# Kernel optimization log

Hardware: AMD Instinct MI355X
Metric: run time of the kernel (lower is better)

Reference implementation:

```python
import jax, jax.numpy as jnp
import numpy as np

B, S, E, H = 4, 2048, 1024, 16
D = E // H  # head_size = 64

def setup_inputs() -> dict:
    key = jax.random.key(0)
    ks = jax.random.split(key, 10)
    s_e = E ** -0.5
    s_4e = (4 * E) ** -0.5
    inp = {
        "x": jax.random.normal(ks[0], (B, S, E), dtype=jnp.float32),
        # per-head Q/K/V weights, stacked: [H, E, D], no bias
        "Wq": jax.random.normal(ks[1], (H, E, D), dtype=jnp.float32) * s_e,
        "Wk": jax.random.normal(ks[2], (H, E, D), dtype=jnp.float32) * s_e,
        "Wv": jax.random.normal(ks[3], (H, E, D), dtype=jnp.float32) * s_e,
        "Wo": jax.random.normal(ks[4], (E, E), dtype=jnp.float32) * s_e,
        "bo": jax.random.normal(ks[5], (E,), dtype=jnp.float32) * 0.01,
        "W1": jax.random.normal(ks[6], (E, 4 * E), dtype=jnp.float32) * s_e,
        "b1": jax.random.normal(ks[7], (4 * E,), dtype=jnp.float32) * 0.01,
        "W2": jax.random.normal(ks[8], (4 * E, E), dtype=jnp.float32) * s_4e,
        "b2": jax.random.normal(ks[9], (E,), dtype=jnp.float32) * 0.01,
    }
    return inp

def reference(x, Wq, Wk, Wv, Wo, bo, W1, b1, W2, b2):
    b, s, e = x.shape
    # NOTE: original scales by embedding_size**-0.5 (Size of x), not head_size
    scale = e ** -0.5
    q = jnp.einsum("bse,hed->bhsd", x, Wq)
    k = jnp.einsum("bse,hed->bhsd", x, Wk)
    v = jnp.einsum("bse,hed->bhsd", x, Wv)
    scores = jnp.einsum("bhsd,bhtd->bhst", q, k) * scale
    causal = jnp.tril(jnp.ones((s, s), dtype=bool))
    scores = jnp.where(causal, scores, -jnp.inf)
    weights = jax.nn.softmax(scores, axis=-1)
    attn = jnp.einsum("bhst,bhtd->bhsd", weights, v)  # [B,H,S,D]
    # concat heads along last dim: [B,S,H*D]
    attn = attn.transpose(0, 2, 1, 3).reshape(b, s, e)
    y = attn @ Wo + bo
    x = x + y  # residual (no LayerNorm applied in original forward)
    h = jax.nn.relu(x @ W1 + b1)
    ffn = h @ W2 + b2
    return x + ffn
```

## Files before the change

kernel.cpp:

```cpp
#include <hip/hip_runtime.h>
#include <stdint.h>

#define B_ 4
#define S_ 2048
#define E_ 1024
#define H_ 16
#define D_ 64

typedef unsigned short u16;
typedef u16 u16x8 __attribute__((ext_vector_type(8)));
typedef __bf16 bf16x8 __attribute__((ext_vector_type(8)));
typedef float f32x4 __attribute__((ext_vector_type(4)));

__device__ __forceinline__ float bf2f(u16 x) {
  unsigned int v = ((unsigned int)x) << 16;
  return __builtin_bit_cast(float, v);
}
__device__ __forceinline__ u16 f2bf(float f) {
  unsigned int u = __builtin_bit_cast(unsigned int, f);
  unsigned int r = (u + 0x7fffu + ((u >> 16) & 1u)) >> 16;
  return (u16)r;
}

__device__ __forceinline__ void gl2lds16(const u16* g, u16* l) {
  __builtin_amdgcn_global_load_lds(
      (const __attribute__((address_space(1))) void*)g,
      (__attribute__((address_space(3))) void*)l, 16, 0, 0);
}

__global__ __launch_bounds__(256) void cast_bf16_k(const float* __restrict__ src,
                                                   u16* __restrict__ dst, long n) {
  long i = ((long)blockIdx.x * 256 + threadIdx.x) * 8;
  if (i + 8 <= n) {
    f32x4 a = *(const f32x4*)(src + i), b = *(const f32x4*)(src + i + 4);
    u16x8 o;
#pragma unroll
    for (int j = 0; j < 4; j++) { o[j] = f2bf(a[j]); o[j + 4] = f2bf(b[j]); }
    *(u16x8*)(dst + i) = o;
  }
}

__global__ __launch_bounds__(256) void castT_k(const float* __restrict__ src,
                                               u16* __restrict__ dst, int R, int C) {
  long bofs = (long)blockIdx.z * R * C;
  src += bofs; dst += bofs;
  __shared__ u16 t[32][33];
  int c0 = blockIdx.x * 32, r0 = blockIdx.y * 32;
  int lc = threadIdx.x & 31, lr8 = threadIdx.x >> 5;
#pragma unroll
  for (int i = 0; i < 4; i++) {
    int lr = lr8 + i * 8;
    t[lr][lc] = f2bf(src[(long)(r0 + lr) * C + c0 + lc]);
  }
  __syncthreads();
#pragma unroll
  for (int i = 0; i < 4; i++) {
    int lr = lr8 + i * 8;
    dst[(long)(c0 + lr) * R + r0 + lc] = t[lc][lr];
  }
}

__global__ __launch_bounds__(256) void vT_k(const u16* __restrict__ QKV,
                                            u16* __restrict__ VTg) {
  int bh = blockIdx.z, d0 = blockIdx.y * 32, t0 = blockIdx.x * 32;
  int b = bh >> 4, h = bh & 15;
  __shared__ u16 t[32][33];
  int lc = threadIdx.x & 31, lr8 = threadIdx.x >> 5;
#pragma unroll
  for (int i = 0; i < 4; i++) {
    int lr = lr8 + i * 8;
    t[lr][lc] = QKV[(long)(b * S_ + t0 + lr) * 3072 + 2048 + h * 64 + d0 + lc];
  }
  __syncthreads();
#pragma unroll
  for (int i = 0; i < 4; i++) {
    int lr = lr8 + i * 8;
    VTg[((long)bh * 64 + d0 + lr) * S_ + t0 + lc] = t[lc][lr];
  }
}

template <bool AF32, bool CF32>
__global__ __launch_bounds__(256) void gemm128(const void* __restrict__ Av,
                                               const u16* __restrict__ BT,
                                               void* __restrict__ Cv,
                                               const float* __restrict__ bias,
                                               const float* __restrict__ resid,
                                               int M, int N, int K, int relu,
                                               u16* __restrict__ Cbf) {
  __shared__ u16 As[128 * 32];
  __shared__ u16 Bs[128 * 32];
  const int tid = threadIdx.x;
  const int wave = tid >> 6, lane = tid & 63;
  const int m0 = blockIdx.y * 128, n0 = blockIdx.x * 128;
  const int wm = wave >> 1, wn = wave & 1;
  const int fr = lane & 15, quad = lane >> 4;

  f32x4 acc[4][4] = {};

  const int srow = wave * 32 + (lane >> 2);
  const int skcol = (lane & 3) * 8;

  for (int k0 = 0; k0 < K; k0 += 32) {
    __syncthreads();
    if (AF32) {
      const float* Ap = (const float*)Av + (long)(m0 + (tid >> 1)) * K + k0 + (tid & 1) * 16;
      f32x4 f0 = *(const f32x4*)Ap, f1 = *(const f32x4*)(Ap + 4);
      f32x4 f2 = *(const f32x4*)(Ap + 8), f3 = *(const f32x4*)(Ap + 12);
      u16x8 p0, p1;
#pragma unroll
      for (int j = 0; j < 4; j++) {
        p0[j] = f2bf(f0[j]); p0[j + 4] = f2bf(f1[j]);
        p1[j] = f2bf(f2[j]); p1[j + 4] = f2bf(f3[j]);
      }
      *(u16x8*)&As[(tid >> 1) * 32 + (tid & 1) * 16] = p0;
      *(u16x8*)&As[(tid >> 1) * 32 + (tid & 1) * 16 + 8] = p1;
    } else {
      const u16* Ag = (const u16*)Av + (long)(m0 + srow) * K + k0 + skcol;
      gl2lds16(Ag, &As[(wave * 32) * 32]);
      gl2lds16(Ag + 16 * (long)K, &As[(wave * 32 + 16) * 32]);
    }
    {
      const u16* Bg = BT + (long)(n0 + srow) * K + k0 + skcol;
      gl2lds16(Bg, &Bs[(wave * 32) * 32]);
      gl2lds16(Bg + 16 * (long)K, &Bs[(wave * 32 + 16) * 32]);
    }
    __syncthreads();

    bf16x8 af[4], bfr[4];
#pragma unroll
    for (int mi = 0; mi < 4; mi++)
      af[mi] = __builtin_bit_cast(bf16x8, *(const u16x8*)&As[(wm * 64 + mi * 16 + fr) * 32 + quad * 8]);
#pragma unroll
    for (int ni = 0; ni < 4; ni++)
      bfr[ni] = __builtin_bit_cast(bf16x8, *(const u16x8*)&Bs[(wn * 64 + ni * 16 + fr) * 32 + quad * 8]);
#pragma unroll
    for (int mi = 0; mi < 4; mi++)
#pragma unroll
      for (int ni = 0; ni < 4; ni++)
        acc[mi][ni] = __builtin_amdgcn_mfma_f32_16x16x32_bf16(af[mi], bfr[ni], acc[mi][ni], 0, 0, 0);
  }

#pragma unroll
  for (int mi = 0; mi < 4; mi++)
#pragma unroll
    for (int ni = 0; ni < 4; ni++)
#pragma unroll
      for (int r = 0; r < 4; r++) {
        int gm = m0 + wm * 64 + mi * 16 + quad * 4 + r;
        int gn = n0 + wn * 64 + ni * 16 + fr;
        float v = acc[mi][ni][r];
        if (bias) v += bias[gn];
        if (resid) v += resid[(long)gm * N + gn];
        if (relu) v = fmaxf(v, 0.f);
        if (CF32) ((float*)Cv)[(long)gm * N + gn] = v;
        else      ((u16*)Cv)[(long)gm * N + gn] = f2bf(v);
        if (Cbf) Cbf[(long)gm * N + gn] = f2bf(v);
      }
}

__device__ __forceinline__ bf16x8 ldfrag32(const u16* base, int r, int quad) {
  int u = (r * 32 + quad * 8) ^ (((r >> 3) & 1) << 4);
  return __builtin_bit_cast(bf16x8, *(const u16x8*)(base + u));
}

__device__ __forceinline__ void stage_tile(const u16* __restrict__ A,
                                           const u16* __restrict__ BT, int K,
                                           int m0, int n0, int k0,
                                           u16* __restrict__ buf,
                                           int sr_, int sc_, int wbase) {
#pragma unroll
  for (int h = 0; h < 2; h++) {
    int r = h * 128 + sr_;
    int c = sc_ ^ (((r >> 3) & 1) << 4);
    gl2lds16(A + (size_t)(m0 + r) * K + k0 + c, buf + h * 4096 + wbase);
  }
  int c = sc_ ^ (((sr_ >> 3) & 1) << 4);
  gl2lds16(BT + (size_t)(n0 + sr_) * K + k0 + c, buf + 8192 + wbase);
}

template <bool CF32>
__global__ __launch_bounds__(512) void gemm3b(const u16* __restrict__ A,
                                              const u16* __restrict__ BT,
                                              void* __restrict__ Cv,
                                              const float* __restrict__ bias,
                                              const float* __restrict__ resid,
                                              int M, int N, int K, int relu,
                                              u16* __restrict__ Cbf) {
  (void)M;
  constexpr int BM = 256, BN = 128, BK = 32;
  constexpr int AU = BM * BK;
  constexpr int BUF = AU + BN * BK;

  __shared__ u16 sm[3 * BUF];
  const int tid = threadIdx.x;
  const int wave = tid >> 6, lane = tid & 63;
  const int wm = wave >> 1, wn = wave & 1;
  const int fr = lane & 15, quad = lane >> 4;

  const int nbx = gridDim.x;
  const int nwg = nbx * (int)gridDim.y;
  const int wgid = blockIdx.y * nbx + blockIdx.x;
  const int qq = nwg >> 3, rr = nwg & 7;
  const int xcd = wgid & 7, loc = wgid >> 3;
  const int sw = (xcd < rr ? xcd * (qq + 1) : rr * (qq + 1) + (xcd - rr) * qq) + loc;
  const int n0 = (sw % nbx) * BN;
  const int m0 = (sw / nbx) * BM;

  const int NT = K / BK;

  f32x4 acc[4][4] = {};

  const int sc_ = (tid & 3) * 8;
  const int sr_ = tid >> 2;
  const int wbase = wave << 9;

  const int rA = wm * 64 + fr;
  const int rB = wn * 64 + fr;

  stage_tile(A, BT, K, m0, n0, 0, sm, sr_, sc_, wbase);
  if (NT > 1) {
    stage_tile(A, BT, K, m0, n0, BK, sm + BUF, sr_, sc_, wbase);
    asm volatile("s_waitcnt vmcnt(3)" ::: "memory");
  } else {
    asm volatile("s_waitcnt vmcnt(0)" ::: "memory");
  }
  __builtin_amdgcn_s_barrier();

  int cur = 0;
  for (int t = 0; t < NT; ++t) {
    u16* cb = sm + cur * BUF;

    if (t + 2 < NT) {
      int s2 = cur + 2; if (s2 >= 3) s2 -= 3;
      stage_tile(A, BT, K, m0, n0, (t + 2) * BK, sm + s2 * BUF, sr_, sc_, wbase);
    }

    bf16x8 aF[4], bF[4];
#pragma unroll
    for (int mi = 0; mi < 4; ++mi) aF[mi] = ldfrag32(cb, rA + mi * 16, quad);
#pragma unroll
    for (int ni = 0; ni < 4; ++ni) bF[ni] = ldfrag32(cb + AU, rB + ni * 16, quad);

    asm volatile("s_waitcnt lgkmcnt(0)" ::: "memory");
    __builtin_amdgcn_sched_barrier(0);
    __builtin_amdgcn_s_setprio(1);
#pragma unroll
    for (int mi = 0; mi < 4; ++mi)
#pragma unroll
      for (int ni = 0; ni < 4; ++ni)
        acc[mi][ni] = __builtin_amdgcn_mfma_f32_16x16x32_bf16(aF[mi], bF[ni], acc[mi][ni], 0, 0, 0);
    __builtin_amdgcn_s_setprio(0);

    if (t + 2 < NT) asm volatile("s_waitcnt vmcnt(3)" ::: "memory");
    else            asm volatile("s_waitcnt vmcnt(0)" ::: "memory");
    __builtin_amdgcn_s_barrier();
    cur = cur + 1; if (cur >= 3) cur -= 3;
  }

#pragma unroll
  for (int mi = 0; mi < 4; ++mi)
#pragma unroll
    for (int ni = 0; ni < 4; ++ni)
#pragma unroll
      for (int r = 0; r < 4; ++r) {
        int gm = m0 + wm * 64 + mi * 16 + quad * 4 + r;
        int gn = n0 + wn * 64 + ni * 16 + fr;
        float v = acc[mi][ni][r];
        if (bias) v += bias[gn];
        if (resid) v += resid[(long)gm * N + gn];
        if (relu) v = fmaxf(v, 0.f);
        if (CF32) ((float*)Cv)[(long)gm * N + gn] = v;
        else      ((u16*)Cv)[(long)gm * N + gn] = f2bf(v);
        if (Cbf) Cbf[(long)gm * N + gn] = f2bf(v);
      }
}

__global__ __launch_bounds__(256) void attn_mfma3(const u16* __restrict__ QKV,
                                                  const u16* __restrict__ VTg,
                                                  u16* __restrict__ attn) {
  int p = blockIdx.x, h = blockIdx.y, b = blockIdx.z;
  int tid = threadIdx.x;
  int wq = tid >> 6, lane = tid & 63;
  int fr = lane & 15, quad = lane >> 4;
  int kf = quad * 8;

  __shared__ u16 Qs[64][72];
  __shared__ u16 Ks[64][72];
  __shared__ u16 Vt[64][72];
  __shared__ u16 Ps[4][16][72];

  const u16* base = QKV + (long)b * S_ * 3072;
  const u16* vbase = VTg + (long)(b * 16 + h) * 64 * S_;
  int st = tid >> 2;
  int sd = (tid & 3) * 16;

  for (int ti = 0; ti < 2; ti++) {
    int qt = ti ? (31 - p) : p;

    {
      const u16* qr = base + (long)(qt * 64 + st) * 3072 + h * 64 + sd;
      u16x8 a = *(const u16x8*)qr, d = *(const u16x8*)(qr + 8);
      u16x8 oa, od;
#pragma unroll
      for (int j = 0; j < 8; j++) {
        oa[j] = f2bf(bf2f(a[j]) * 0.03125f);
        od[j] = f2bf(bf2f(d[j]) * 0.03125f);
      }
      *(u16x8*)&Qs[st][sd] = oa;
      *(u16x8*)&Qs[st][sd + 8] = od;
    }
    __syncthreads();
    bf16x8 qf0 = __builtin_bit_cast(bf16x8, *(const u16x8*)&Qs[wq * 16 + fr][kf]);
    bf16x8 qf1 = __builtin_bit_cast(bf16x8, *(const u16x8*)&Qs[wq * 16 + fr][32 + kf]);

    f32x4 acc[4] = {};
    float l[4] = {0.f, 0.f, 0.f, 0.f};

    for (int c = 0; c <= qt; c++) {
      int t0 = c * 64;
      __syncthreads();
      {
        const u16* kr = base + (long)(t0 + st) * 3072 + 1024 + h * 64 + sd;
        u16x8 k0 = *(const u16x8*)kr, k1 = *(const u16x8*)(kr + 8);
        const u16* vr = vbase + (long)st * S_ + t0 + sd;
        u16x8 v0 = *(const u16x8*)vr, v1 = *(const u16x8*)(vr + 8);
        *(u16x8*)&Ks[st][sd] = k0;
        *(u16x8*)&Ks[st][sd + 8] = k1;
        *(u16x8*)&Vt[st][sd] = v0;
        *(u16x8*)&Vt[st][sd + 8] = v1;
      }
      __syncthreads();

      f32x4 sc[4] = {};
#pragma unroll
      for (int nt = 0; nt < 4; nt++) {
        bf16x8 b0 = __builtin_bit_cast(bf16x8, *(const u16x8*)&Ks[nt * 16 + fr][kf]);
        bf16x8 b1 = __builtin_bit_cast(bf16x8, *(const u16x8*)&Ks[nt * 16 + fr][32 + kf]);
        sc[nt] = __builtin_amdgcn_mfma_f32_16x16x32_bf16(qf0, b0, sc[nt], 0, 0, 0);
        sc[nt] = __builtin_amdgcn_mfma_f32_16x16x32_bf16(qf1, b1, sc[nt], 0, 0, 0);
      }

      if (c == qt) {
        int qloc = wq * 16 + quad * 4;
#pragma unroll
        for (int nt = 0; nt < 4; nt++)
#pragma unroll
          for (int r = 0; r < 4; r++)
            if (nt * 16 + fr > qloc + r) sc[nt][r] = -1e30f;
      }

#pragma unroll
      for (int nt = 0; nt < 4; nt++)
#pragma unroll
        for (int r = 0; r < 4; r++) {
          float pv = __expf(sc[nt][r]);
          sc[nt][r] = pv;
          l[r] += pv;
        }

#pragma unroll
      for (int nt = 0; nt < 4; nt++)
#pragma unroll
        for (int r = 0; r < 4; r++)
          Ps[wq][quad * 4 + r][nt * 16 + fr] = f2bf(sc[nt][r]);

      bf16x8 pa0 = __builtin_bit_cast(bf16x8, *(const u16x8*)&Ps[wq][fr][kf]);
      bf16x8 pa1 = __builtin_bit_cast(bf16x8, *(const u16x8*)&Ps[wq][fr][32 + kf]);
#pragma unroll
      for (int nt = 0; nt < 4; nt++) {
        bf16x8 vb0 = __builtin_bit_cast(bf16x8, *(const u16x8*)&Vt[nt * 16 + fr][kf]);
        bf16x8 vb1 = __builtin_bit_cast(bf16x8, *(const u16x8*)&Vt[nt * 16 + fr][32 + kf]);
        acc[nt] = __builtin_amdgcn_mfma_f32_16x16x32_bf16(pa0, vb0, acc[nt], 0, 0, 0);
        acc[nt] = __builtin_amdgcn_mfma_f32_16x16x32_bf16(pa1, vb1, acc[nt], 0, 0, 0);
      }
    }

#pragma unroll
    for (int r = 0; r < 4; r++)
#pragma unroll
      for (int off = 1; off < 16; off <<= 1) l[r] += __shfl_xor(l[r], off);

    long row = (long)b * S_ + qt * 64 + wq * 16 + quad * 4;
#pragma unroll
    for (int nt = 0; nt < 4; nt++)
#pragma unroll
      for (int r = 0; r < 4; r++)
        attn[(row + r) * 1024 + h * 64 + nt * 16 + fr] = f2bf(acc[nt][r] / l[r]);
  }
}

extern "C" void kernel_launch(void* const* d_in, const int* in_sizes, int n_in,
                              void* d_out, int out_size, void* d_ws, size_t ws_size,
                              hipStream_t stream) {
  (void)in_sizes; (void)n_in; (void)out_size;
  const float* x  = (const float*)d_in[0];
  const float* Wq = (const float*)d_in[1];
  const float* Wk = (const float*)d_in[2];
  const float* Wv = (const float*)d_in[3];
  const float* Wo = (const float*)d_in[4];
  const float* bo = (const float*)d_in[5];
  const float* W1 = (const float*)d_in[6];
  const float* b1 = (const float*)d_in[7];
  const float* W2 = (const float*)d_in[8];
  const float* b2 = (const float*)d_in[9];
  float* out = (float*)d_out;

  char* ws = (char*)d_ws;
  u16*   QKV  = (u16*)(ws);
  u16*   attn = (u16*)(ws + 50331648);
  u16*   hbuf = (u16*)(ws);
  float* x1   = (float*)(ws + 67108864);
  u16*   VTg  = (u16*)(ws + 67108864);
  u16*   xb   = (u16*)(ws + 83886080);
  u16*   WT   = (u16*)(ws + 100663296);
  u16*   WoT  = (u16*)(ws + 106954752);
  u16*   W1T  = (u16*)(ws + 109051904);
  u16*   W2T  = (u16*)(ws + 117440512);
  u16*   x1b  = (u16*)(ws + 125829120);
  bool bigws = ws_size >= (size_t)142606336;

  cast_bf16_k<<<4096, 256, 0, stream>>>(x, xb, (long)8192 * 1024);
  castT_k<<<dim3(2, 32, 16), 256, 0, stream>>>(Wq, WT, 1024, 64);
  castT_k<<<dim3(2, 32, 16), 256, 0, stream>>>(Wk, WT + 1048576, 1024, 64);
  castT_k<<<dim3(2, 32, 16), 256, 0, stream>>>(Wv, WT + 2097152, 1024, 64);
  castT_k<<<dim3(32, 32, 1), 256, 0, stream>>>(Wo, WoT, 1024, 1024);
  castT_k<<<dim3(128, 32, 1), 256, 0, stream>>>(W1, W1T, 1024, 4096);
  castT_k<<<dim3(32, 128, 1), 256, 0, stream>>>(W2, W2T, 4096, 1024);

  gemm3b<false><<<dim3(24, 32), 512, 0, stream>>>(xb, WT, QKV, nullptr, nullptr, 8192, 3072, 1024, 0, nullptr);
  vT_k<<<dim3(64, 2, 64), 256, 0, stream>>>(QKV, VTg);
  attn_mfma3<<<dim3(16, H_, B_), 256, 0, stream>>>(QKV, VTg, attn);
  gemm3b<true><<<dim3(8, 32), 512, 0, stream>>>(attn, WoT, x1, bo, x, 8192, 1024, 1024, 0, bigws ? x1b : nullptr);
  if (bigws)
    gemm3b<false><<<dim3(32, 32), 512, 0, stream>>>(x1b, W1T, hbuf, b1, nullptr, 8192, 4096, 1024, 1, nullptr);
  else
    gemm128<true, false><<<dim3(32, 64), 256, 0, stream>>>(x1, W1T, hbuf, b1, nullptr, 8192, 4096, 1024, 1, nullptr);
  gemm3b<true><<<dim3(8, 32), 512, 0, stream>>>(hbuf, W2T, out, b2, x1, 8192, 1024, 4096, 0, nullptr);
}
```

Baseline: 534.4 us.

## Add 128x128 triple-buffered GEMM and swizzle attention LDS with exp2 softmax

Adds a new 256-thread GEMM kernel with 128x128 tiles, BK=32, triple-buffered async global-to-LDS staging, XCD-aware block remapping and an XOR-swizzled LDS layout. It replaces the 512-thread gemm3b for the QKV, output-projection and W2 GEMMs, giving more, smaller workgroups. The attention kernel switches from padded LDS arrays to XOR-swizzled 64-wide rows to avoid bank conflicts, and folds log2(e) into the Q scale so exp2f can be used. It also fuses the P store into the exp loop. The smaller tiles trade per-block data reuse for higher occupancy and better load balance.

```diff
diff --git a/kernel.cpp b/kernel.cpp
--- a/kernel.cpp
+++ b/kernel.cpp
@@ -275,6 +275,124 @@
       }
 }
 
+__device__ __forceinline__ void stage_tile_s(const u16* __restrict__ A,
+                                             const u16* __restrict__ BT, int K,
+                                             int m0, int n0, int k0,
+                                             u16* __restrict__ buf,
+                                             int sr_, int sc_, int wbase) {
+#pragma unroll
+  for (int h = 0; h < 2; h++) {
+    int r = h * 64 + sr_;
+    int c = sc_ ^ (((r >> 3) & 1) << 4);
+    gl2lds16(A + (size_t)(m0 + r) * K + k0 + c, buf + h * 2048 + wbase);
+  }
+#pragma unroll
+  for (int h = 0; h < 2; h++) {
+    int r = h * 64 + sr_;
+    int c = sc_ ^ (((r >> 3) & 1) << 4);
+    gl2lds16(BT + (size_t)(n0 + r) * K + k0 + c, buf + 4096 + h * 2048 + wbase);
+  }
+}
+
+template <bool CF32>
+__global__ __launch_bounds__(256) void gemm3s(const u16* __restrict__ A,
+                                              const u16* __restrict__ BT,
+                                              void* __restrict__ Cv,
+                                              const float* __restrict__ bias,
+                                              const float* __restrict__ resid,
+                                              int M, int N, int K, int relu,
+                                              u16* __restrict__ Cbf) {
+  (void)M;
+  constexpr int BM = 128, BN = 128, BK = 32;
+  constexpr int AU = BM * BK;
+  constexpr int BUF = 2 * AU;
+
+  __shared__ u16 sm[3 * BUF];
+  const int tid = threadIdx.x;
+  const int wave = tid >> 6, lane = tid & 63;
+  const int wm = wave >> 1, wn = wave & 1;
+  const int fr = lane & 15, quad = lane >> 4;
+
+  const int nbx = gridDim.x;
+  const int nwg = nbx * (int)gridDim.y;
+  const int wgid = blockIdx.y * nbx + blockIdx.x;
+  const int qq = nwg >> 3, rr = nwg & 7;
+  const int xcd = wgid & 7, loc = wgid >> 3;
+  const int sw = (xcd < rr ? xcd * (qq + 1) : rr * (qq + 1) + (xcd - rr) * qq) + loc;
+  const int n0 = (sw % nbx) * BN;
+  const int m0 = (sw / nbx) * BM;
+
+  const int NT = K / BK;
+
+  f32x4 acc[4][4] = {};
+
+  const int sc_ = (tid & 3) * 8;
+  const int sr_ = tid >> 2;
+  const int wbase = wave << 9;
+
+  const int rA = wm * 64 + fr;
+  const int rB = wn * 64 + fr;
+
+  stage_tile_s(A, BT, K, m0, n0, 0, sm, sr_, sc_, wbase);
+  if (NT > 1) {
+    stage_tile_s(A, BT, K, m0, n0, BK, sm + BUF, sr_, sc_, wbase);
+    asm volatile("s_waitcnt vmcnt(4)" ::: "memory");
+  } else {
+    asm volatile("s_waitcnt vmcnt(0)" ::: "memory");
+  }
+  __builtin_amdgcn_s_barrier();
+
+  int cur = 0;
+  for (int t = 0; t < NT; ++t) {
+    u16* cb = sm + cur * BUF;
+
+    if (t + 2 < NT) {
+      int s2 = cur + 2; if (s2 >= 3) s2 -= 3;
+      stage_tile_s(A, BT, K, m0, n0, (t + 2) * BK, sm + s2 * BUF, sr_, sc_, wbase);
+    }
+
+    bf16x8 aF[4], bF[4];
+#pragma unroll
+    for (int mi = 0; mi < 4; ++mi) aF[mi] = ldfrag32(cb, rA + mi * 16, quad);
+#pragma unroll
+    for (int ni = 0; ni < 4; ++ni) bF[ni] = ldfrag32(cb + AU, rB + ni * 16, quad);
+
+    asm volatile("s_waitcnt lgkmcnt(0)" ::: "memory");
+    __builtin_amdgcn_sched_barrier(0);
+    __builtin_amdgcn_s_setprio(1);
+#pragma unroll
+    for (int mi = 0; mi < 4; ++mi)
+#pragma unroll
+      for (int ni = 0; ni < 4; ++ni)
+        acc[mi][ni] = __builtin_amdgcn_mfma_f32_16x16x32_bf16(aF[mi], bF[ni], acc[mi][ni], 0, 0, 0);
+    __builtin_amdgcn_s_setprio(0);
+
+    if (t + 2 < NT) asm volatile("s_waitcnt vmcnt(4)" ::: "memory");
+    else            asm volatile("s_waitcnt vmcnt(0)" ::: "memory");
+    __builtin_amdgcn_s_barrier();
+    cur = cur + 1; if (cur >= 3) cur -= 3;
+  }
+
+#pragma unroll
+  for (int mi = 0; mi < 4; ++mi)
+#pragma unroll
+    for (int ni = 0; ni < 4; ++ni)
+#pragma unroll
+      for (int r = 0; r < 4; ++r) {
+        int gm = m0 + wm * 64 + mi * 16 + quad * 4 + r;
+        int gn = n0 + wn * 64 + ni * 16 + fr;
+        float v = acc[mi][ni][r];
+        if (bias) v += bias[gn];
+        if (resid) v += resid[(long)gm * N + gn];
+        if (relu) v = fmaxf(v, 0.f);
+        if (CF32) ((float*)Cv)[(long)gm * N + gn] = v;
+        else      ((u16*)Cv)[(long)gm * N + gn] = f2bf(v);
+        if (Cbf) Cbf[(long)gm * N + gn] = f2bf(v);
+      }
+}
+
+#define SWZ(row, col) ((((row) << 6)) + ((col) ^ (((row) & 7) << 3)))
+
 __global__ __launch_bounds__(256) void attn_mfma3(const u16* __restrict__ QKV,
                                                   const u16* __restrict__ VTg,
                                                   u16* __restrict__ attn) {
@@ -284,16 +402,18 @@
   int fr = lane & 15, quad = lane >> 4;
   int kf = quad * 8;
 
-  __shared__ u16 Qs[64][72];
-  __shared__ u16 Ks[64][72];
-  __shared__ u16 Vt[64][72];
-  __shared__ u16 Ps[4][16][72];
+  __shared__ u16 Qs[64 * 64];
+  __shared__ u16 Ks[64 * 64];
+  __shared__ u16 Vt[64 * 64];
+  __shared__ u16 Ps[4 * 16 * 64];
 
   const u16* base = QKV + (long)b * S_ * 3072;
   const u16* vbase = VTg + (long)(b * 16 + h) * 64 * S_;
   int st = tid >> 2;
   int sd = (tid & 3) * 16;
 
+  const float qsc = 0.03125f * 1.4426950408889634f;
+
   for (int ti = 0; ti < 2; ti++) {
     int qt = ti ? (31 - p) : p;
 
@@ -303,15 +423,15 @@
       u16x8 oa, od;
 #pragma unroll
       for (int j = 0; j < 8; j++) {
-        oa[j] = f2bf(bf2f(a[j]) * 0.03125f);
-        od[j] = f2bf(bf2f(d[j]) * 0.03125f);
-      }
-      *(u16x8*)&Qs[st][sd] = oa;
-      *(u16x8*)&Qs[st][sd + 8] = od;
+        oa[j] = f2bf(bf2f(a[j]) * qsc);
+        od[j] = f2bf(bf2f(d[j]) * qsc);
+      }
+      *(u16x8*)&Qs[SWZ(st, sd)] = oa;
+      *(u16x8*)&Qs[SWZ(st, sd + 8)] = od;
     }
     __syncthreads();
-    bf16x8 qf0 = __builtin_bit_cast(bf16x8, *(const u16x8*)&Qs[wq * 16 + fr][kf]);
-    bf16x8 qf1 = __builtin_bit_cast(bf16x8, *(const u16x8*)&Qs[wq * 16 + fr][32 + kf]);
+    bf16x8 qf0 = __builtin_bit_cast(bf16x8, *(const u16x8*)&Qs[SWZ(wq * 16 + fr, kf)]);
+    bf16x8 qf1 = __builtin_bit_cast(bf16x8, *(const u16x8*)&Qs[SWZ(wq * 16 + fr, 32 + kf)]);
 
     f32x4 acc[4] = {};
     float l[4] = {0.f, 0.f, 0.f, 0.f};
@@ -324,18 +444,18 @@
         u16x8 k0 = *(const u16x8*)kr, k1 = *(const u16x8*)(kr + 8);
         const u16* vr = vbase + (long)st * S_ + t0 + sd;
         u16x8 v0 = *(const u16x8*)vr, v1 = *(const u16x8*)(vr + 8);
-        *(u16x8*)&Ks[st][sd] = k0;
-        *(u16x8*)&Ks[st][sd + 8] = k1;
-        *(u16x8*)&Vt[st][sd] = v0;
-        *(u16x8*)&Vt[st][sd + 8] = v1;
+        *(u16x8*)&Ks[SWZ(st, sd)] = k0;
+        *(u16x8*)&Ks[SWZ(st, sd + 8)] = k1;
+        *(u16x8*)&Vt[SWZ(st, sd)] = v0;
+        *(u16x8*)&Vt[SWZ(st, sd + 8)] = v1;
       }
       __syncthreads();
 
       f32x4 sc[4] = {};
 #pragma unroll
       for (int nt = 0; nt < 4; nt++) {
-        bf16x8 b0 = __builtin_bit_cast(bf16x8, *(const u16x8*)&Ks[nt * 16 + fr][kf]);
-        bf16x8 b1 = __builtin_bit_cast(bf16x8, *(const u16x8*)&Ks[nt * 16 + fr][32 + kf]);
+        bf16x8 b0 = __builtin_bit_cast(bf16x8, *(const u16x8*)&Ks[SWZ(nt * 16 + fr, kf)]);
+        bf16x8 b1 = __builtin_bit_cast(bf16x8, *(const u16x8*)&Ks[SWZ(nt * 16 + fr, 32 + kf)]);
         sc[nt] = __builtin_amdgcn_mfma_f32_16x16x32_bf16(qf0, b0, sc[nt], 0, 0, 0);
         sc[nt] = __builtin_amdgcn_mfma_f32_16x16x32_bf16(qf1, b1, sc[nt], 0, 0, 0);
       }
@@ -349,27 +469,25 @@
             if (nt * 16 + fr > qloc + r) sc[nt][r] = -1e30f;
       }
 
-#pragma unroll
-      for (int nt = 0; nt < 4; nt++)
+      const int pb = wq << 10;
+      const int prow = quad * 4;
+#pragma unroll
+      for (int nt = 0; nt < 4; nt++) {
+        int col = nt * 16 + fr;
 #pragma unroll
         for (int r = 0; r < 4; r++) {
-          float pv = __expf(sc[nt][r]);
-          sc[nt][r] = pv;
+          float pv = exp2f(sc[nt][r]);
           l[r] += pv;
+          Ps[pb + SWZ(prow + r, col)] = f2bf(pv);
         }
-
-#pragma unroll
-      for (int nt = 0; nt < 4; nt++)
-#pragma unroll
-        for (int r = 0; r < 4; r++)
-          Ps[wq][quad * 4 + r][nt * 16 + fr] = f2bf(sc[nt][r]);
-
-      bf16x8 pa0 = __builtin_bit_cast(bf16x8, *(const u16x8*)&Ps[wq][fr][kf]);
-      bf16x8 pa1 = __builtin_bit_cast(bf16x8, *(const u16x8*)&Ps[wq][fr][32 + kf]);
+      }
+
+      bf16x8 pa0 = __builtin_bit_cast(bf16x8, *(const u16x8*)&Ps[pb + SWZ(fr, kf)]);
+      bf16x8 pa1 = __builtin_bit_cast(bf16x8, *(const u16x8*)&Ps[pb + SWZ(fr, 32 + kf)]);
 #pragma unroll
       for (int nt = 0; nt < 4; nt++) {
-        bf16x8 vb0 = __builtin_bit_cast(bf16x8, *(const u16x8*)&Vt[nt * 16 + fr][kf]);
-        bf16x8 vb1 = __builtin_bit_cast(bf16x8, *(const u16x8*)&Vt[nt * 16 + fr][32 + kf]);
+        bf16x8 vb0 = __builtin_bit_cast(bf16x8, *(const u16x8*)&Vt[SWZ(nt * 16 + fr, kf)]);
+        bf16x8 vb1 = __builtin_bit_cast(bf16x8, *(const u16x8*)&Vt[SWZ(nt * 16 + fr, 32 + kf)]);
         acc[nt] = __builtin_amdgcn_mfma_f32_16x16x32_bf16(pa0, vb0, acc[nt], 0, 0, 0);
         acc[nt] = __builtin_amdgcn_mfma_f32_16x16x32_bf16(pa1, vb1, acc[nt], 0, 0, 0);
       }
@@ -427,13 +545,13 @@
   castT_k<<<dim3(128, 32, 1), 256, 0, stream>>>(W1, W1T, 1024, 4096);
   castT_k<<<dim3(32, 128, 1), 256, 0, stream>>>(W2, W2T, 4096, 1024);
 
-  gemm3b<false><<<dim3(24, 32), 512, 0, stream>>>(xb, WT, QKV, nullptr, nullptr, 8192, 3072, 1024, 0, nullptr);
+  gemm3s<false><<<dim3(24, 64), 256, 0, stream>>>(xb, WT, QKV, nullptr, nullptr, 8192, 3072, 1024, 0, nullptr);
   vT_k<<<dim3(64, 2, 64), 256, 0, stream>>>(QKV, VTg);
   attn_mfma3<<<dim3(16, H_, B_), 256, 0, stream>>>(QKV, VTg, attn);
-  gemm3b<true><<<dim3(8, 32), 512, 0, stream>>>(attn, WoT, x1, bo, x, 8192, 1024, 1024, 0, bigws ? x1b : nullptr);
+  gemm3s<true><<<dim3(8, 64), 256, 0, stream>>>(attn, WoT, x1, bo, x, 8192, 1024, 1024, 0, bigws ? x1b : nullptr);
   if (bigws)
     gemm3b<false><<<dim3(32, 32), 512, 0, stream>>>(x1b, W1T, hbuf, b1, nullptr, 8192, 4096, 1024, 1, nullptr);
   else
     gemm128<true, false><<<dim3(32, 64), 256, 0, stream>>>(x1, W1T, hbuf, b1, nullptr, 8192, 4096, 1024, 1, nullptr);
-  gemm3b<true><<<dim3(8, 32), 512, 0, stream>>>(hbuf, W2T, out, b2, x1, 8192, 1024, 4096, 0, nullptr);
-}
+  gemm3s<true><<<dim3(8, 64), 256, 0, stream>>>(hbuf, W2T, out, b2, x1, 8192, 1024, 4096, 0, nullptr);
+}
```

Result: slower. 569.1 us (+6.5%).

## Double-buffer K/V tiles with register prefetch and use exp2 softmax in attention

Applied to the files above, without the earlier changes.

The attention kernel now prefetches the next K/V chunk into registers while the current chunk is processed, and double-buffers the K and V tiles in LDS so that each iteration needs one barrier instead of two. The Q scale absorbs log2(e) so the softmax can use exp2f instead of __expf. The Q staging buffer is reused as the per-wave P buffer to save LDS. Each thread holds more registers for the prefetch, which could reduce occupancy.

```diff
diff --git a/kernel.cpp b/kernel.cpp
--- a/kernel.cpp
+++ b/kernel.cpp
@@ -275,7 +275,7 @@
       }
 }
 
-__global__ __launch_bounds__(256) void attn_mfma3(const u16* __restrict__ QKV,
+__global__ __launch_bounds__(256) void attn_mfma4(const u16* __restrict__ QKV,
                                                   const u16* __restrict__ VTg,
                                                   u16* __restrict__ attn) {
   int p = blockIdx.x, h = blockIdx.y, b = blockIdx.z;
@@ -284,18 +284,30 @@
   int fr = lane & 15, quad = lane >> 4;
   int kf = quad * 8;
 
-  __shared__ u16 Qs[64][72];
-  __shared__ u16 Ks[64][72];
-  __shared__ u16 Vt[64][72];
-  __shared__ u16 Ps[4][16][72];
+  __shared__ u16 Ks[2][64][72];
+  __shared__ u16 Vt[2][64][72];
+  __shared__ u16 QP[64 * 72];
 
   const u16* base = QKV + (long)b * S_ * 3072;
   const u16* vbase = VTg + (long)(b * 16 + h) * 64 * S_;
   int st = tid >> 2;
   int sd = (tid & 3) * 16;
 
+  const float qsc = 0.03125f * 1.4426950408889634f;
+  u16* Pw = QP + wq * (16 * 72);
+
   for (int ti = 0; ti < 2; ti++) {
     int qt = ti ? (31 - p) : p;
+
+    __syncthreads();
+
+    u16x8 ck0, ck1, cv0, cv1;
+    {
+      const u16* kr = base + (long)st * 3072 + 1024 + h * 64 + sd;
+      ck0 = *(const u16x8*)kr; ck1 = *(const u16x8*)(kr + 8);
+      const u16* vr = vbase + (long)st * S_ + sd;
+      cv0 = *(const u16x8*)vr; cv1 = *(const u16x8*)(vr + 8);
+    }
 
     {
       const u16* qr = base + (long)(qt * 64 + st) * 3072 + h * 64 + sd;
@@ -303,39 +315,39 @@
       u16x8 oa, od;
 #pragma unroll
       for (int j = 0; j < 8; j++) {
-        oa[j] = f2bf(bf2f(a[j]) * 0.03125f);
-        od[j] = f2bf(bf2f(d[j]) * 0.03125f);
-      }
-      *(u16x8*)&Qs[st][sd] = oa;
-      *(u16x8*)&Qs[st][sd + 8] = od;
+        oa[j] = f2bf(bf2f(a[j]) * qsc);
+        od[j] = f2bf(bf2f(d[j]) * qsc);
+      }
+      *(u16x8*)&QP[st * 72 + sd] = oa;
+      *(u16x8*)&QP[st * 72 + sd + 8] = od;
     }
     __syncthreads();
-    bf16x8 qf0 = __builtin_bit_cast(bf16x8, *(const u16x8*)&Qs[wq * 16 + fr][kf]);
-    bf16x8 qf1 = __builtin_bit_cast(bf16x8, *(const u16x8*)&Qs[wq * 16 + fr][32 + kf]);
+    bf16x8 qf0 = __builtin_bit_cast(bf16x8, *(const u16x8*)&QP[(wq * 16 + fr) * 72 + kf]);
+    bf16x8 qf1 = __builtin_bit_cast(bf16x8, *(const u16x8*)&QP[(wq * 16 + fr) * 72 + 32 + kf]);
 
     f32x4 acc[4] = {};
     float l[4] = {0.f, 0.f, 0.f, 0.f};
 
     for (int c = 0; c <= qt; c++) {
-      int t0 = c * 64;
+      int bi = c & 1;
+      *(u16x8*)&Ks[bi][st][sd] = ck0;
+      *(u16x8*)&Ks[bi][st][sd + 8] = ck1;
+      *(u16x8*)&Vt[bi][st][sd] = cv0;
+      *(u16x8*)&Vt[bi][st][sd + 8] = cv1;
+      if (c < qt) {
+        int t0n = (c + 1) * 64;
+        const u16* kr = base + (long)(t0n + st) * 3072 + 1024 + h * 64 + sd;
+        ck0 = *(const u16x8*)kr; ck1 = *(const u16x8*)(kr + 8);
+        const u16* vr = vbase + (long)st * S_ + t0n + sd;
+        cv0 = *(const u16x8*)vr; cv1 = *(const u16x8*)(vr + 8);
+      }
       __syncthreads();
-      {
-        const u16* kr = base + (long)(t0 + st) * 3072 + 1024 + h * 64 + sd;
-        u16x8 k0 = *(const u16x8*)kr, k1 = *(const u16x8*)(kr + 8);
-        const u16* vr = vbase + (long)st * S_ + t0 + sd;
-        u16x8 v0 = *(const u16x8*)vr, v1 = *(const u16x8*)(vr + 8);
-        *(u16x8*)&Ks[st][sd] = k0;
-        *(u16x8*)&Ks[st][sd + 8] = k1;
-        *(u16x8*)&Vt[st][sd] = v0;
-        *(u16x8*)&Vt[st][sd + 8] = v1;
-      }
-      __syncthreads();
 
       f32x4 sc[4] = {};
 #pragma unroll
       for (int nt = 0; nt < 4; nt++) {
-        bf16x8 b0 = __builtin_bit_cast(bf16x8, *(const u16x8*)&Ks[nt * 16 + fr][kf]);
-        bf16x8 b1 = __builtin_bit_cast(bf16x8, *(const u16x8*)&Ks[nt * 16 + fr][32 + kf]);
+        bf16x8 b0 = __builtin_bit_cast(bf16x8, *(const u16x8*)&Ks[bi][nt * 16 + fr][kf]);
+        bf16x8 b1 = __builtin_bit_cast(bf16x8, *(const u16x8*)&Ks[bi][nt * 16 + fr][32 + kf]);
         sc[nt] = __builtin_amdgcn_mfma_f32_16x16x32_bf16(qf0, b0, sc[nt], 0, 0, 0);
         sc[nt] = __builtin_amdgcn_mfma_f32_16x16x32_bf16(qf1, b1, sc[nt], 0, 0, 0);
       }
@@ -349,27 +361,24 @@
             if (nt * 16 + fr > qloc + r) sc[nt][r] = -1e30f;
       }
 
-#pragma unroll
-      for (int nt = 0; nt < 4; nt++)
+      const int prow = quad * 4;
+#pragma unroll
+      for (int nt = 0; nt < 4; nt++) {
+        int col = nt * 16 + fr;
 #pragma unroll
         for (int r = 0; r < 4; r++) {
-          float pv = __expf(sc[nt][r]);
-          sc[nt][r] = pv;
+          float pv = exp2f(sc[nt][r]);
           l[r] += pv;
+          Pw[(prow + r) * 72 + col] = f2bf(pv);
         }
-
-#pragma unroll
-      for (int nt = 0; nt < 4; nt++)
-#pragma unroll
-        for (int r = 0; r < 4; r++)
-          Ps[wq][quad * 4 + r][nt * 16 + fr] = f2bf(sc[nt][r]);
-
-      bf16x8 pa0 = __builtin_bit_cast(bf16x8, *(const u16x8*)&Ps[wq][fr][kf]);
-      bf16x8 pa1 = __builtin_bit_cast(bf16x8, *(const u16x8*)&Ps[wq][fr][32 + kf]);
+      }
+
+      bf16x8 pa0 = __builtin_bit_cast(bf16x8, *(const u16x8*)&Pw[fr * 72 + kf]);
+      bf16x8 pa1 = __builtin_bit_cast(bf16x8, *(const u16x8*)&Pw[fr * 72 + 32 + kf]);
 #pragma unroll
       for (int nt = 0; nt < 4; nt++) {
-        bf16x8 vb0 = __builtin_bit_cast(bf16x8, *(const u16x8*)&Vt[nt * 16 + fr][kf]);
-        bf16x8 vb1 = __builtin_bit_cast(bf16x8, *(const u16x8*)&Vt[nt * 16 + fr][32 + kf]);
+        bf16x8 vb0 = __builtin_bit_cast(bf16x8, *(const u16x8*)&Vt[bi][nt * 16 + fr][kf]);
+        bf16x8 vb1 = __builtin_bit_cast(bf16x8, *(const u16x8*)&Vt[bi][nt * 16 + fr][32 + kf]);
         acc[nt] = __builtin_amdgcn_mfma_f32_16x16x32_bf16(pa0, vb0, acc[nt], 0, 0, 0);
         acc[nt] = __builtin_amdgcn_mfma_f32_16x16x32_bf16(pa1, vb1, acc[nt], 0, 0, 0);
       }
@@ -429,7 +438,7 @@
 
   gemm3b<false><<<dim3(24, 32), 512, 0, stream>>>(xb, WT, QKV, nullptr, nullptr, 8192, 3072, 1024, 0, nullptr);
   vT_k<<<dim3(64, 2, 64), 256, 0, stream>>>(QKV, VTg);
-  attn_mfma3<<<dim3(16, H_, B_), 256, 0, stream>>>(QKV, VTg, attn);
+  attn_mfma4<<<dim3(16, H_, B_), 256, 0, stream>>>(QKV, VTg, attn);
   gemm3b<true><<<dim3(8, 32), 512, 0, stream>>>(attn, WoT, x1, bo, x, 8192, 1024, 1024, 0, bigws ? x1b : nullptr);
   if (bigws)
     gemm3b<false><<<dim3(32, 32), 512, 0, stream>>>(x1b, W1T, hbuf, b1, nullptr, 8192, 4096, 1024, 1, nullptr);
```

Measured after the change: 538.8 us. Within noise of the previous version (+0.8%).
